# Performance work log

Hardware: AMD Instinct MI355X
Metric: run time of the kernel (lower is better)

The kernel has to match this reference:

```python
import jax, jax.numpy as jnp
import numpy as np

BN_EPS = 1e-5  # torch BatchNorm1d default


def setup_inputs() -> dict:
    key = jax.random.key(0)
    ks = jax.random.split(key, 4)
    B, C, N, O = 8, 64, 4096, 64
    x = jax.random.normal(ks[0], (B, C, N, 1), dtype=jnp.float32)
    w1 = jax.random.normal(ks[1], (C, O), dtype=jnp.float32) * (1.0 / np.sqrt(C))
    b1 = jnp.zeros((O,), jnp.float32)
    gamma = jnp.ones((O,), jnp.float32)
    beta = jnp.zeros((O,), jnp.float32)
    w2 = jax.random.normal(ks[2], (O, O), dtype=jnp.float32) * (1.0 / np.sqrt(O))
    b2 = jnp.zeros((O,), jnp.float32)
    eps_gin = jnp.zeros((), jnp.float32)  # train_eps=True, init eps=0.0
    return {"x": x, "w1": w1, "b1": b1, "gamma": gamma, "beta": beta,
            "w2": w2, "b2": b2, "eps_gin": eps_gin, "k": 16}


def _knn_idx(xf, k):
    # xf: [B, N, C] -> indices of k nearest neighbors (incl. self, loop=True)
    sq = jnp.sum(xf * xf, axis=-1)                       # [B, N]
    d = sq[:, :, None] + sq[:, None, :] - 2.0 * jnp.einsum('bnc,bmc->bnm', xf, xf)
    _, idx = jax.lax.top_k(-d, k)                        # [B, N, k]
    return idx


def reference(x, w1, b1, gamma, beta, w2, b2, eps_gin, k):
    B, C, N, _ = x.shape
    xf = jnp.transpose(x[..., 0], (0, 2, 1))             # [B, N, C]
    idx = _knn_idx(xf, k)                                # [B, N, k]
    # GIN aggregation: each node has exactly k neighbors -> gather + sum
    gathered = jax.vmap(lambda xb, ib: xb[ib])(xf, idx)  # [B, N, k, C]
    aggr = gathered.sum(axis=2)                          # [B, N, C]
    h = (1.0 + eps_gin) * xf + aggr                      # [B, N, C]
    hf = h.reshape(B * N, C)
    h1 = hf @ w1 + b1                                    # [B*N, O]
    # BatchNorm1d, training-mode batch statistics (biased variance)
    mean = jnp.mean(h1, axis=0)
    var = jnp.mean((h1 - mean) ** 2, axis=0)
    hn = gamma * (h1 - mean) / jnp.sqrt(var + BN_EPS) + beta
    hg = jax.nn.gelu(hn, approximate=False)              # torch default GELU (erf)
    out = hg @ w2 + b2                                   # [B*N, O]
    return jnp.transpose(out.reshape(B, N, -1), (0, 2, 1))[..., None]  # [B, O, N, 1]
```

## Files before the change

### kernel.cpp

```cpp
#include <hip/hip_runtime.h>
#include <cstdint>
#include <cstddef>

#define B_ 8
#define C_ 64
#define N_ 4096
#define O_ 64
#define ROWS_ (B_*N_)
#define NSPLIT_ 2
#define CAPB_ 33
#define TAU_TILES_ 8
#define MIDROWS_ 16
#define FINROWS_ 32

typedef unsigned long long u64;
typedef unsigned int u32;
typedef unsigned short u16;
typedef __attribute__((ext_vector_type(8))) short bf16x8;
typedef __attribute__((ext_vector_type(16))) float f32x16;

#define MFMA32(A,Bv,Cv) __builtin_amdgcn_mfma_f32_32x32x16_bf16(A,Bv,Cv,0,0,0)

#define OFF_XF   0
#define OFF_SQ   8388608
#define OFF_KD   8519680
#define OFF_KI   16908288
#define OFF_PACK 21102592
#define OFF_H1   21102592
#define OFF_BN   33685504

__device__ __forceinline__ void insert16(u64 kv[16], u64 key) {
  if (key < kv[15]) {
#pragma unroll
    for (int j = 15; j > 0; --j) {
      u64 a = kv[j-1], b = kv[j];
      kv[j] = (key < a) ? a : ((key < b) ? key : b);
    }
    kv[0] = (key < kv[0]) ? key : kv[0];
  }
}

__global__ __launch_bounds__(256) void k_transpose(const float* __restrict__ x,
                                                   float* __restrict__ xf,
                                                   float* __restrict__ sq,
                                                   u16* __restrict__ pack) {
  __shared__ float lds[64 * 33];
  const int b  = blockIdx.x >> 7;
  const int nt = blockIdx.x & 127;
  const int n0 = nt << 5;
  const int tid = threadIdx.x;
  const float* xb = x + (size_t)b * C_ * N_;
  {
    const int nn = tid & 31;
    const int c0 = tid >> 5;
#pragma unroll
    for (int i = 0; i < 8; ++i) {
      int c = c0 + i * 8;
      lds[c * 33 + nn] = xb[(size_t)c * N_ + n0 + nn];
    }
  }
  __syncthreads();
  {
    const int cc  = tid & 63;
    const int nn0 = tid >> 6;
#pragma unroll
    for (int i = 0; i < 8; ++i) {
      int nn = nn0 + i * 4;
      xf[((size_t)(b * N_ + n0 + nn)) * 64 + cc] = lds[cc * 33 + nn];
    }
  }
  if (tid < 32) {
    float s = 0.f;
#pragma unroll
    for (int c = 0; c < 64; ++c) { float v = lds[c * 33 + tid]; s += v * v; }
    sq[b * N_ + n0 + tid] = s;
  }
  {
    const int lane = tid & 63;
    const int slice = tid >> 6;
    const int kb = slice * 16 + (lane >> 5) * 8;
    const int nl = lane & 31;
    bf16x8 H, M, L;
#pragma unroll
    for (int j = 0; j < 8; ++j) {
      float f = lds[(kb + j) * 33 + nl];
      u32 u = __float_as_uint(f);
      u32 rh = (u + 0x7FFFu + ((u >> 16) & 1u)) >> 16;
      float bh = __uint_as_float(rh << 16);
      float f1 = f - bh;
      u = __float_as_uint(f1);
      u32 rm = (u + 0x7FFFu + ((u >> 16) & 1u)) >> 16;
      float bm = __uint_as_float(rm << 16);
      float f2 = f1 - bm;
      u = __float_as_uint(f2);
      u32 rl = (u + 0x7FFFu + ((u >> 16) & 1u)) >> 16;
      H[j] = (short)rh; M[j] = (short)rm; L[j] = (short)rl;
    }
    u16* basep = pack + ((size_t)(b * 128 + nt) * 12) * 512 + lane * 8;
    *(bf16x8*)(basep + (size_t)(0 + slice) * 512) = H;
    *(bf16x8*)(basep + (size_t)(4 + slice) * 512) = M;
    *(bf16x8*)(basep + (size_t)(8 + slice) * 512) = L;
  }
}

#define KNN_LOAD(P, mt) do { const u16* ap_ = pb + (size_t)(mt) * (12*512); \
  P##h0 = *(const bf16x8*)(ap_ + 0*512);  P##h1 = *(const bf16x8*)(ap_ + 1*512); \
  P##h2 = *(const bf16x8*)(ap_ + 2*512);  P##h3 = *(const bf16x8*)(ap_ + 3*512); \
  P##m0 = *(const bf16x8*)(ap_ + 4*512);  P##m1 = *(const bf16x8*)(ap_ + 5*512); \
  P##m2 = *(const bf16x8*)(ap_ + 6*512);  P##m3 = *(const bf16x8*)(ap_ + 7*512); \
  P##l0 = *(const bf16x8*)(ap_ + 8*512);  P##l1 = *(const bf16x8*)(ap_ + 9*512); \
  P##l2 = *(const bf16x8*)(ap_ +10*512);  P##l3 = *(const bf16x8*)(ap_ +11*512); } while(0)

#define SQ_LOAD(MT) do { const float* sp_ = sqb + (MT) * 32 + 4 * h; \
  sv0 = *(const float4*)(sp_);      sv1 = *(const float4*)(sp_ + 8); \
  sv2 = *(const float4*)(sp_ + 16); sv3 = *(const float4*)(sp_ + 24); } while(0)

#define KNN_MFMA(P) \
  acc0 = MFMA32(P##h0, ql0, acc0);  acc1 = MFMA32(P##h1, ql1, acc1); \
  acc0 = MFMA32(P##l0, qh0, acc0);  acc1 = MFMA32(P##l1, qh1, acc1); \
  acc0 = MFMA32(P##m0, qm0, acc0);  acc1 = MFMA32(P##m1, qm1, acc1); \
  acc0 = MFMA32(P##h0, qm0, acc0);  acc1 = MFMA32(P##h1, qm1, acc1); \
  acc0 = MFMA32(P##m0, qh0, acc0);  acc1 = MFMA32(P##m1, qh1, acc1); \
  acc0 = MFMA32(P##h0, qh0, acc0);  acc1 = MFMA32(P##h1, qh1, acc1); \
  acc0 = MFMA32(P##h2, ql2, acc0);  acc1 = MFMA32(P##h3, ql3, acc1); \
  acc0 = MFMA32(P##l2, qh2, acc0);  acc1 = MFMA32(P##l3, qh3, acc1); \
  acc0 = MFMA32(P##m2, qm2, acc0);  acc1 = MFMA32(P##m3, qm3, acc1); \
  acc0 = MFMA32(P##h2, qm2, acc0);  acc1 = MFMA32(P##h3, qm3, acc1); \
  acc0 = MFMA32(P##m2, qh2, acc0);  acc1 = MFMA32(P##m3, qh3, acc1); \
  acc0 = MFMA32(P##h2, qh2, acc0);  acc1 = MFMA32(P##h3, qh3, acc1);

#define SEL_T8() do { \
  float sqv_[16] = {sv0.x, sv0.y, sv0.z, sv0.w, sv1.x, sv1.y, sv1.z, sv1.w, \
                    sv2.x, sv2.y, sv2.z, sv2.w, sv3.x, sv3.y, sv3.z, sv3.w}; \
_Pragma("unroll") \
  for (int r_ = 0; r_ < 16; ++r_) { \
    float d_ = fmaf(-2.f, acc0[r_] + acc1[r_], sqv_[r_]); \
    if (d_ < kv1[7]) { \
_Pragma("unroll") \
      for (int j_ = 7; j_ > 0; --j_) { \
        float a_ = kv1[j_-1], b_ = kv1[j_]; \
        kv1[j_] = (d_ < a_) ? a_ : ((d_ < b_) ? d_ : b_); \
      } \
      kv1[0] = (d_ < kv1[0]) ? d_ : kv1[0]; \
    } \
  } \
} while(0)

#define SEL_C(MT) do { \
  const u32 ic_ = (u32)((MT) * 32 + 4 * h); \
  float sqv_[16] = {sv0.x, sv0.y, sv0.z, sv0.w, sv1.x, sv1.y, sv1.z, sv1.w, \
                    sv2.x, sv2.y, sv2.z, sv2.w, sv3.x, sv3.y, sv3.z, sv3.w}; \
_Pragma("unroll") \
  for (int r_ = 0; r_ < 16; ++r_) { \
    float d_ = fmaf(-2.f, acc0[r_] + acc1[r_], sqv_[r_]); \
    if (d_ <= tauF) { \
      u32 u_ = __float_as_uint(d_); \
      u_ ^= ((int)u_ < 0) ? 0xFFFFFFFFu : 0x80000000u; \
      myc[cnt] = ((u64)u_ << 32) | (u64)(ic_ + (u32)((r_ & 3) + 8 * (r_ >> 2))); \
      ++cnt; \
    } \
  } \
  if (__any(cnt >= CAPB_ - 16)) {             \
    for (int i_ = 0; i_ < cnt; ++i_) insert16(kv, myc[i_]); \
    cnt = 0; \
  } \
} while(0)

__global__ __launch_bounds__(256, 2) void k_knn(const u16* __restrict__ pack,
                                                const float* __restrict__ sq,
                                                u32* __restrict__ kd,
                                                u16* __restrict__ ki,
                                                float* __restrict__ bn_acc) {
  __shared__ u64 cand[256 * CAPB_];
  const int bx = blockIdx.x;
  const int tid = threadIdx.x;
  if (bx == 0 && tid < 128) bn_acc[tid] = 0.f;
  const int split = bx & 1;
  const int qb = (bx >> 1) & 31;
  const int b = bx >> 6;
  const int lane = tid & 63;
  const int wid = tid >> 6;
  const int qt = qb * 4 + wid;
  const int h = lane >> 5;
  const u16* pb = pack + (size_t)b * (128 * 12 * 512) + lane * 8;

  const u16* qp = pb + (size_t)qt * (12 * 512);
  bf16x8 qh0 = *(const bf16x8*)(qp + 0*512), qh1 = *(const bf16x8*)(qp + 1*512);
  bf16x8 qh2 = *(const bf16x8*)(qp + 2*512), qh3 = *(const bf16x8*)(qp + 3*512);
  bf16x8 qm0 = *(const bf16x8*)(qp + 4*512), qm1 = *(const bf16x8*)(qp + 5*512);
  bf16x8 qm2 = *(const bf16x8*)(qp + 6*512), qm3 = *(const bf16x8*)(qp + 7*512);
  bf16x8 ql0 = *(const bf16x8*)(qp + 8*512), ql1 = *(const bf16x8*)(qp + 9*512);
  bf16x8 ql2 = *(const bf16x8*)(qp + 10*512), ql3 = *(const bf16x8*)(qp + 11*512);

  const float* sqb = sq + b * N_;
  const int mbase = split * 64;

  bf16x8 Ah0, Ah1, Ah2, Ah3, Am0, Am1, Am2, Am3, Al0, Al1, Al2, Al3;
  bf16x8 Bh0, Bh1, Bh2, Bh3, Bm0, Bm1, Bm2, Bm3, Bl0, Bl1, Bl2, Bl3;
  float4 sv0, sv1, sv2, sv3;

  float kv1[8];
#pragma unroll
  for (int j = 0; j < 8; ++j) kv1[j] = __uint_as_float(0x7F800000u);

  KNN_LOAD(A, mbase);
  for (int ct = 0; ct < TAU_TILES_; ct += 2) {
    SQ_LOAD(mbase + ct);
    KNN_LOAD(B, mbase + ct + 1);
    {
      f32x16 acc0 = {0,0,0,0,0,0,0,0,0,0,0,0,0,0,0,0};
      f32x16 acc1 = {0,0,0,0,0,0,0,0,0,0,0,0,0,0,0,0};
      KNN_MFMA(A)
      SEL_T8();
    }
    SQ_LOAD(mbase + ct + 1);
    KNN_LOAD(A, mbase + ct + 2);
    {
      f32x16 acc0 = {0,0,0,0,0,0,0,0,0,0,0,0,0,0,0,0};
      f32x16 acc1 = {0,0,0,0,0,0,0,0,0,0,0,0,0,0,0,0};
      KNN_MFMA(B)
      SEL_T8();
    }
  }
  float tkF = kv1[7];
  float pkF = __shfl_xor(tkF, 32);
  const float tauF = (tkF > pkF) ? tkF : pkF;

  u64 kv[16];
#pragma unroll
  for (int j = 0; j < 16; ++j) kv[j] = 0xFF8000000000FFFFull;
  int cnt = 0;
  u64* myc = cand + tid * CAPB_;

  KNN_LOAD(A, mbase);
  for (int ct = 0; ct < 64; ct += 2) {
    SQ_LOAD(mbase + ct);
    KNN_LOAD(B, mbase + ct + 1);
    {
      f32x16 acc0 = {0,0,0,0,0,0,0,0,0,0,0,0,0,0,0,0};
      f32x16 acc1 = {0,0,0,0,0,0,0,0,0,0,0,0,0,0,0,0};
      KNN_MFMA(A)
      SEL_C(mbase + ct);
    }
    SQ_LOAD(mbase + ct + 1);
    KNN_LOAD(A, mbase + ((ct + 2) & 63));
    {
      f32x16 acc0 = {0,0,0,0,0,0,0,0,0,0,0,0,0,0,0,0};
      f32x16 acc1 = {0,0,0,0,0,0,0,0,0,0,0,0,0,0,0,0};
      KNN_MFMA(B)
      SEL_C(mbase + ct + 1);
    }
  }
  for (int i = 0; i < cnt; ++i) insert16(kv, myc[i]);

  u64 m[16];
#pragma unroll
  for (int j = 0; j < 16; ++j) {
    u64 p = __shfl_xor(kv[15 - j], 32);
    m[j] = (kv[j] < p) ? kv[j] : p;
  }
#pragma unroll
  for (int d = 8; d >= 1; d >>= 1) {
#pragma unroll
    for (int j = 0; j < 16; ++j) {
      if ((j & d) == 0) {
        u64 a = m[j], c = m[j | d];
        m[j] = (a < c) ? a : c;
        m[j | d] = (a < c) ? c : a;
      }
    }
  }

  if (lane < 32) {
    const int row = b * N_ + qt * 32 + lane;
    u32* dp = kd + ((size_t)row * NSPLIT_ + split) * 16;
    u16* ip = ki + ((size_t)row * NSPLIT_ + split) * 16;
#pragma unroll
    for (int j = 0; j < 16; ++j) {
      dp[j] = (u32)(m[j] >> 32);
      ip[j] = (u16)(m[j] & 0xFFFFu);
    }
  }
}

__global__ __launch_bounds__(256) void k_mid(const u32* __restrict__ kd,
                                             const u16* __restrict__ ki,
                                             const float* __restrict__ xf,
                                             const float* __restrict__ eps_gin,
                                             const float* __restrict__ w1,
                                             const float* __restrict__ b1,
                                             float* __restrict__ h1,
                                             float* __restrict__ bn_acc) {
  __shared__ float wT[64 * 65];
  __shared__ float hL[MIDROWS_ * 68];
  __shared__ int   knnL[MIDROWS_ * 16];
  __shared__ float rs[4][64], rs2[4][64];
  const int tid = threadIdx.x;
  const int r0 = blockIdx.x * MIDROWS_;
#pragma unroll
  for (int i = 0; i < 16; ++i) {
    int idx = tid + i * 256;
    wT[(idx & 63) * 65 + (idx >> 6)] = w1[idx];
  }
  {
    const int row = tid >> 4;
    const int j = tid & 15;
    const u32* dp = kd + (size_t)(r0 + row) * (NSPLIT_ * 16);
    const u16* ip = ki + (size_t)(r0 + row) * (NSPLIT_ * 16);
    u64 a = ((u64)dp[j] << 32) | ip[j];
    u64 bb = ((u64)dp[16 + (15 - j)] << 32) | ip[16 + (15 - j)];
    knnL[row * 16 + j] = (int)((a < bb ? a : bb) & 0xFFFFu);
  }
  __syncthreads();
  const int q = tid >> 6;
  const int b = r0 >> 12;
  const float* xfb = xf + (size_t)b * N_ * 64;
  const float eps1 = 1.f + eps_gin[0];
  {
    const int lane = tid & 63;
    const int rg = lane >> 4;
    const int ch = (lane & 15) * 4;
    const int rl = q * 4 + rg;
    float4 v = *(const float4*)&xfb[(size_t)((r0 & (N_ - 1)) + rl) * 64 + ch];
    v.x *= eps1; v.y *= eps1; v.z *= eps1; v.w *= eps1;
    const int* kn = knnL + rl * 16;
#pragma unroll
    for (int j = 0; j < 16; ++j) {
      int mr = kn[j];
      float4 g = *(const float4*)&xfb[(size_t)mr * 64 + ch];
      v.x += g.x; v.y += g.y; v.z += g.z; v.w += g.w;
    }
    *(float4*)&hL[rl * 68 + ch] = v;
  }
  __syncthreads();
  const int o = tid & 63;
  const float bias = b1[o];
  float s = 0.f, s2 = 0.f;
#pragma unroll
  for (int i = 0; i < 4; ++i) {
    int rl = q * 4 + i;
    float acc = bias;
#pragma unroll
    for (int k = 0; k < 16; ++k) {
      float4 hv = *(const float4*)&hL[rl * 68 + 4 * k];
      float4 wv = *(const float4*)&wT[o * 65 + 4 * k];
      acc += hv.x * wv.x; acc += hv.y * wv.y;
      acc += hv.z * wv.z; acc += hv.w * wv.w;
    }
    h1[(size_t)(r0 + rl) * 64 + o] = acc;
    s += acc; s2 += acc * acc;
  }
  rs[q][o] = s; rs2[q][o] = s2;
  __syncthreads();
  if (tid < 64) {
    float ts  = rs[0][tid] + rs[1][tid] + rs[2][tid] + rs[3][tid];
    float ts2 = rs2[0][tid] + rs2[1][tid] + rs2[2][tid] + rs2[3][tid];
    atomicAdd(&bn_acc[tid], ts);
    atomicAdd(&bn_acc[64 + tid], ts2);
  }
}

__global__ __launch_bounds__(256) void k_final(const float* __restrict__ h1,
                                               const float* __restrict__ bn_acc,
                                               const float* __restrict__ gamma,
                                               const float* __restrict__ beta,
                                               const float* __restrict__ w2,
                                               const float* __restrict__ b2,
                                               float* __restrict__ out) {
  __shared__ float wT2[64 * 65];
  __shared__ float hg[FINROWS_ * 65];
  __shared__ float scsh[128];
  const int tid = threadIdx.x;
#pragma unroll
  for (int i = 0; i < 16; ++i) {
    int idx = tid + i * 256;
    wT2[(idx & 63) * 65 + (idx >> 6)] = w2[idx];
  }
  if (tid < 64) {
    const float inv = 1.f / (float)ROWS_;
    float mean = bn_acc[tid] * inv;
    float var  = bn_acc[64 + tid] * inv - mean * mean;
    float sc = gamma[tid] * rsqrtf(var + 1e-5f);
    scsh[tid] = sc;
    scsh[64 + tid] = beta[tid] - mean * sc;
  }
  __syncthreads();
  const int r0 = blockIdx.x * FINROWS_;
  const int b  = r0 >> 12;
  const int n0 = r0 & (N_ - 1);
  const int o = tid & 63;
  const int q = tid >> 6;
  const float sc = scsh[o], sh = scsh[64 + o];
#pragma unroll
  for (int i = 0; i < 8; ++i) {
    int rl = q + i * 4;
    float v = h1[(size_t)(r0 + rl) * 64 + o] * sc + sh;
    float g = 0.5f * v * (1.f + erff(v * 0.70710678118654752f));
    hg[rl * 65 + o] = g;
  }
  __syncthreads();
  const int nl = tid & 31;
  const int g8 = tid >> 5;
  float4 hv[16];
#pragma unroll
  for (int k = 0; k < 16; ++k) hv[k] = *(const float4*)&hg[nl * 65 + 4 * k];
#pragma unroll
  for (int i = 0; i < 8; ++i) {
    int o2 = g8 * 8 + i;
    float acc = b2[o2];
#pragma unroll
    for (int k = 0; k < 16; ++k) {
      float4 wv = *(const float4*)&wT2[o2 * 65 + 4 * k];
      acc += hv[k].x * wv.x; acc += hv[k].y * wv.y;
      acc += hv[k].z * wv.z; acc += hv[k].w * wv.w;
    }
    out[((size_t)(b * 64 + o2)) * N_ + n0 + nl] = acc;
  }
}

extern "C" void kernel_launch(void* const* d_in, const int* in_sizes, int n_in,
                              void* d_out, int out_size, void* d_ws, size_t ws_size,
                              hipStream_t stream) {
  const float* x     = (const float*)d_in[0];
  const float* w1    = (const float*)d_in[1];
  const float* b1    = (const float*)d_in[2];
  const float* gamma = (const float*)d_in[3];
  const float* beta  = (const float*)d_in[4];
  const float* w2    = (const float*)d_in[5];
  const float* b2    = (const float*)d_in[6];
  const float* eps_g = (const float*)d_in[7];
  float* out = (float*)d_out;

  char* ws = (char*)d_ws;
  float* xf   = (float*)(ws + OFF_XF);
  float* sq   = (float*)(ws + OFF_SQ);
  u32*   kd   = (u32*)  (ws + OFF_KD);
  u16*   ki   = (u16*)  (ws + OFF_KI);
  u16*   pack = (u16*)  (ws + OFF_PACK);
  float* h1   = (float*)(ws + OFF_H1);
  float* bn_acc = (float*)(ws + OFF_BN);

  k_transpose<<<1024, 256, 0, stream>>>(x, xf, sq, pack);
  k_knn<<<512, 256, 0, stream>>>(pack, sq, kd, ki, bn_acc);
  k_mid<<<ROWS_ / MIDROWS_, 256, 0, stream>>>(kd, ki, xf, eps_g, w1, b1, h1, bn_acc);
  k_final<<<ROWS_ / FINROWS_, 256, 0, stream>>>(h1, bn_acc, gamma, beta, w2, b2, out);
}
```

Measured before the change: 332.6 us.

## Fuse tau-estimation pass into candidate scan and tighten threshold adaptively

```diff
diff --git a/kernel.cpp b/kernel.cpp
--- a/kernel.cpp
+++ b/kernel.cpp
@@ -129,12 +129,27 @@
   acc0 = MFMA32(P##m2, qh2, acc0);  acc1 = MFMA32(P##m3, qh3, acc1); \
   acc0 = MFMA32(P##h2, qh2, acc0);  acc1 = MFMA32(P##h3, qh3, acc1);
 
-#define SEL_T8() do { \
+#define DRAINC() do { \
+  for (int i_ = 0; i_ < cnt; ++i_) insert16(kv, myc[i_]); \
+  cnt = 0; \
+  u32 k15_ = (u32)(kv[15] >> 32); \
+  float f15_ = __uint_as_float((k15_ & 0x80000000u) ? (k15_ ^ 0x80000000u) : ~k15_); \
+  thresh = (thresh < f15_) ? thresh : f15_; \
+} while(0)
+
+#define SEL_TC(MT) do { \
+  const u32 ic_ = (u32)((MT) * 32 + 4 * h); \
   float sqv_[16] = {sv0.x, sv0.y, sv0.z, sv0.w, sv1.x, sv1.y, sv1.z, sv1.w, \
                     sv2.x, sv2.y, sv2.z, sv2.w, sv3.x, sv3.y, sv3.z, sv3.w}; \
 _Pragma("unroll") \
   for (int r_ = 0; r_ < 16; ++r_) { \
     float d_ = fmaf(-2.f, acc0[r_] + acc1[r_], sqv_[r_]); \
+    if (d_ <= thresh) { \
+      u32 u_ = __float_as_uint(d_); \
+      u_ ^= ((int)u_ < 0) ? 0xFFFFFFFFu : 0x80000000u; \
+      myc[cnt] = ((u64)u_ << 32) | (u64)(ic_ + (u32)((r_ & 3) + 8 * (r_ >> 2))); \
+      ++cnt; \
+    } \
     if (d_ < kv1[7]) { \
 _Pragma("unroll") \
       for (int j_ = 7; j_ > 0; --j_) { \
@@ -144,6 +159,11 @@
       kv1[0] = (d_ < kv1[0]) ? d_ : kv1[0]; \
     } \
   } \
+  if (__any(cnt >= CAPB_ - 16)) DRAINC(); \
+  { float tk_ = kv1[7]; \
+    float pk_ = __shfl_xor(tk_, 32); \
+    float tr_ = (tk_ > pk_) ? tk_ : pk_; \
+    thresh = (thresh < tr_) ? thresh : tr_; } \
 } while(0)
 
 #define SEL_C(MT) do { \
@@ -153,17 +173,14 @@
 _Pragma("unroll") \
   for (int r_ = 0; r_ < 16; ++r_) { \
     float d_ = fmaf(-2.f, acc0[r_] + acc1[r_], sqv_[r_]); \
-    if (d_ <= tauF) { \
+    if (d_ <= thresh) { \
       u32 u_ = __float_as_uint(d_); \
       u_ ^= ((int)u_ < 0) ? 0xFFFFFFFFu : 0x80000000u; \
       myc[cnt] = ((u64)u_ << 32) | (u64)(ic_ + (u32)((r_ & 3) + 8 * (r_ >> 2))); \
       ++cnt; \
     } \
   } \
-  if (__any(cnt >= CAPB_ - 16)) {             \
-    for (int i_ = 0; i_ < cnt; ++i_) insert16(kv, myc[i_]); \
-    cnt = 0; \
-  } \
+  if (__any(cnt >= CAPB_ - 16)) DRAINC(); \
 } while(0)
 
 __global__ __launch_bounds__(256, 2) void k_knn(const u16* __restrict__ pack,
@@ -202,6 +219,12 @@
   float kv1[8];
 #pragma unroll
   for (int j = 0; j < 8; ++j) kv1[j] = __uint_as_float(0x7F800000u);
+  u64 kv[16];
+#pragma unroll
+  for (int j = 0; j < 16; ++j) kv[j] = 0xFF8000000000FFFFull;
+  int cnt = 0;
+  u64* myc = cand + tid * CAPB_;
+  float thresh = __uint_as_float(0x7F800000u);
 
   KNN_LOAD(A, mbase);
   for (int ct = 0; ct < TAU_TILES_; ct += 2) {
@@ -211,7 +234,7 @@
       f32x16 acc0 = {0,0,0,0,0,0,0,0,0,0,0,0,0,0,0,0};
       f32x16 acc1 = {0,0,0,0,0,0,0,0,0,0,0,0,0,0,0,0};
       KNN_MFMA(A)
-      SEL_T8();
+      SEL_TC(mbase + ct);
     }
     SQ_LOAD(mbase + ct + 1);
     KNN_LOAD(A, mbase + ct + 2);
@@ -219,21 +242,11 @@
       f32x16 acc0 = {0,0,0,0,0,0,0,0,0,0,0,0,0,0,0,0};
       f32x16 acc1 = {0,0,0,0,0,0,0,0,0,0,0,0,0,0,0,0};
       KNN_MFMA(B)
-      SEL_T8();
-    }
-  }
-  float tkF = kv1[7];
-  float pkF = __shfl_xor(tkF, 32);
-  const float tauF = (tkF > pkF) ? tkF : pkF;
-
-  u64 kv[16];
-#pragma unroll
-  for (int j = 0; j < 16; ++j) kv[j] = 0xFF8000000000FFFFull;
-  int cnt = 0;
-  u64* myc = cand + tid * CAPB_;
-
-  KNN_LOAD(A, mbase);
-  for (int ct = 0; ct < 64; ct += 2) {
+      SEL_TC(mbase + ct + 1);
+    }
+  }
+
+  for (int ct = TAU_TILES_; ct < 64; ct += 2) {
     SQ_LOAD(mbase + ct);
     KNN_LOAD(B, mbase + ct + 1);
     {
```

Result: no change. 338.0 us (+1.6%).
